# Optimization experiments

Hardware: AMD Instinct MI355X
Metric: run time of the kernel (lower is better)

The kernel has to match this reference:

```python
import jax, jax.numpy as jnp
import numpy as np

NUM_EXPERTS = 8
TOP_K = 2

def setup_inputs() -> dict:
    key = jax.random.key(0)
    k1, k2, k3, k4 = jax.random.split(key, 4)
    B, T, C, F = 4, 2048, 1024, 4096
    x = jax.random.normal(k1, (B, T, C), dtype=jnp.float32)
    gate_w = jax.random.normal(k2, (C, NUM_EXPERTS), dtype=jnp.float32) * 0.02
    w1 = jax.random.normal(k3, (NUM_EXPERTS, C, F), dtype=jnp.float32) * 0.02
    w2 = jax.random.normal(k4, (NUM_EXPERTS, F, C), dtype=jnp.float32) * 0.02
    return {"x": x, "gate_w": gate_w, "w1": w1, "w2": w2}

def reference(x, gate_w, w1, w2):
    # Router: softmax over experts, then top-k and renormalize
    router_logits = jnp.einsum('btc,ce->bte', x, gate_w)          # [B,T,E]
    routing = jax.nn.softmax(router_logits, axis=-1)
    topw, topi = jax.lax.top_k(routing, TOP_K)                    # [B,T,K]
    topw = topw / jnp.sum(topw, axis=-1, keepdims=True)
    # Combined per-expert weight per token (zero if not selected)
    onehot = jax.nn.one_hot(topi, NUM_EXPERTS, dtype=x.dtype)     # [B,T,K,E]
    combine = jnp.einsum('btk,btke->bte', topw, onehot)           # [B,T,E]
    # Expert FFNs (exact GELU, matching torch nn.GELU default)
    out = jnp.zeros_like(x)
    for e in range(NUM_EXPERTS):
        h = jax.nn.gelu(jnp.einsum('btc,cf->btf', x, w1[e]), approximate=False)
        y = jnp.einsum('btf,fc->btc', h, w2[e])
        out = out + combine[..., e:e+1] * y
    return out
```

## Files before the change

kernel.cpp:

```cpp
#include <hip/hip_runtime.h>
#include <hip/hip_bf16.h>
#include <math.h>

#define NUM_EXPERTS 8
#define NTOK 8192
#define CDIM 1024
#define FDIM 4096
#define MAXSLOTS 17408
#define MAXTILES 136

typedef __bf16 bf16x8 __attribute__((ext_vector_type(8)));
typedef float  f32x4  __attribute__((ext_vector_type(4)));

#define GPTR(p) ((const __attribute__((address_space(1))) unsigned int*)(p))
#define LPTR(p) ((__attribute__((address_space(3))) unsigned int*)(p))

__device__ __forceinline__ float gelu_exact(float v){
  return 0.5f * v * (1.0f + erff(v * 0.70710678118654752f));
}

__global__ __launch_bounds__(256) void moe_router(
    const float* __restrict__ x, const float* __restrict__ gw,
    int2* __restrict__ topi, float2* __restrict__ topw, int* __restrict__ counts)
{
  int token = blockIdx.x * 4 + (threadIdx.x >> 6);
  int lane  = threadIdx.x & 63;
  int e = lane & 7, part = lane >> 3;
  const float* xr = x + (size_t)token * CDIM;
  float s = 0.f;
  int c0 = part * 128;
  for (int c = c0; c < c0 + 128; ++c) s += xr[c] * gw[c * 8 + e];
  s += __shfl_xor(s, 8); s += __shfl_xor(s, 16); s += __shfl_xor(s, 32);
  float m1 = s; int i1 = e;
  for (int off = 1; off < 8; off <<= 1){
    float ov = __shfl_xor(m1, off); int oi = __shfl_xor(i1, off);
    if (ov > m1 || (ov == m1 && oi < i1)){ m1 = ov; i1 = oi; }
  }
  float l2 = (e == i1) ? -INFINITY : s;
  float m2 = l2; int i2 = e;
  for (int off = 1; off < 8; off <<= 1){
    float ov = __shfl_xor(m2, off); int oi = __shfl_xor(i2, off);
    if (ov > m2 || (ov == m2 && oi < i2)){ m2 = ov; i2 = oi; }
  }
  if (lane == 0){
    float r = expf(m2 - m1);
    float wa = 1.f / (1.f + r);
    topi[token] = make_int2(i1, i2);
    topw[token] = make_float2(wa, 1.f - wa);
    atomicAdd(&counts[i1], 1);
    atomicAdd(&counts[i2], 1);
  }
}

__global__ __launch_bounds__(256) void convert_x_kernel(
    const float* __restrict__ x, __hip_bfloat16* __restrict__ xb)
{
  int i = (blockIdx.x * 256 + threadIdx.x) * 4;
  float4 v = *(const float4*)(x + i);
  union { __hip_bfloat16 hh[4]; ushort4 u; } cv;
  cv.hh[0] = __float2bfloat16(v.x);
  cv.hh[1] = __float2bfloat16(v.y);
  cv.hh[2] = __float2bfloat16(v.z);
  cv.hh[3] = __float2bfloat16(v.w);
  *(ushort4*)(xb + i) = cv.u;
}

__global__ __launch_bounds__(256) void transpose_bf16_kernel(
    const float* __restrict__ in, __hip_bfloat16* __restrict__ outp, int R, int Cc)
{
  __shared__ float tile[32][33];
  const size_t msz = (size_t)R * Cc;
  const float* inm = in + (size_t)blockIdx.z * msz;
  __hip_bfloat16* outm = outp + (size_t)blockIdx.z * msz;
  int r0 = blockIdx.y * 32, c0 = blockIdx.x * 32;
  int tx = threadIdx.x, ty = threadIdx.y;
  for (int yy = 0; yy < 32; yy += 8)
    tile[ty + yy][tx] = inm[(size_t)(r0 + ty + yy) * Cc + c0 + tx];
  __syncthreads();
  for (int yy = 0; yy < 32; yy += 8)
    outm[(size_t)(c0 + ty + yy) * R + r0 + tx] = __float2bfloat16(tile[tx][ty + yy]);
}

__global__ void scan_kernel(const int* __restrict__ counts, int* cursors, int* num_tiles,
    int* tile_expert, int* tile_slotbase, int* slot_token, float* slot_weight)
{
  int t = threadIdx.x;
  if (t == 0){
    int base = 0, T = 0;
    for (int e = 0; e < NUM_EXPERTS; ++e){
      cursors[e] = base;
      int nt = (counts[e] + 127) >> 7;
      for (int i = 0; i < nt; ++i){ tile_expert[T] = e; tile_slotbase[T] = base + i * 128; ++T; }
      base += nt << 7;
    }
    *num_tiles = T;
  }
  for (int i = t; i < MAXSLOTS; i += 256){ slot_token[i] = 0; slot_weight[i] = 0.f; }
}

__global__ void assign_kernel(const int2* __restrict__ topi, const float2* __restrict__ topw,
    int* cursors, int* slot_token, float* slot_weight)
{
  int token = blockIdx.x * 256 + threadIdx.x;
  int2 ii = topi[token];
  float2 ww = topw[token];
  int p0 = atomicAdd(&cursors[ii.x], 1);
  slot_token[p0] = token; slot_weight[p0] = ww.x;
  int p1 = atomicAdd(&cursors[ii.y], 1);
  slot_token[p1] = token; slot_weight[p1] = ww.y;
}

__global__ __launch_bounds__(256) void gemm1_kernel(
    const __hip_bfloat16* __restrict__ xbf, const __hip_bfloat16* __restrict__ w1t,
    __hip_bfloat16* __restrict__ h, const int* __restrict__ num_tiles,
    const int* __restrict__ tile_expert, const int* __restrict__ tile_slotbase,
    const int* __restrict__ slot_token)
{
  __shared__ __align__(16) __hip_bfloat16 As[128 * 64];
  __shared__ __align__(16) __hip_bfloat16 Bs[128 * 64];
  const int tm = blockIdx.y;
  if (tm >= *num_tiles) return;
  const int e = tile_expert[tm];
  const int sbase = tile_slotbase[tm];
  const int n0 = blockIdx.x * 128;
  const int t = threadIdx.x;
  const int cl = t & 7;
  const __hip_bfloat16* w1e = w1t + (size_t)e * FDIM * CDIM;
  const __hip_bfloat16* aptr[4];
  const __hip_bfloat16* bptr[4];
#pragma unroll
  for (int j = 0; j < 4; ++j){
    int r = j * 32 + (t >> 3);
    int cg = cl ^ (r & 7);
    int tok = slot_token[sbase + r];
    aptr[j] = xbf + (size_t)tok * CDIM + cg * 8;
    bptr[j] = w1e + (size_t)(n0 + r) * CDIM + cg * 8;
  }
  char* asml = (char*)As + t * 16;
  char* bsml = (char*)Bs + t * 16;

  f32x4 acc[4][4] = {};
  const int lane = t & 63, wv = t >> 6;
  const int wm = (wv >> 1) * 64, wn = (wv & 1) * 64;
  const int lrow = lane & 15, quad = lane >> 4;

  for (int k0 = 0; k0 < CDIM; k0 += 64){
    __syncthreads();
#pragma unroll
    for (int j = 0; j < 4; ++j){
      __builtin_amdgcn_global_load_lds(GPTR(aptr[j] + k0), LPTR(asml + j * 4096), 16, 0, 0);
      __builtin_amdgcn_global_load_lds(GPTR(bptr[j] + k0), LPTR(bsml + j * 4096), 16, 0, 0);
    }
    __syncthreads();
#pragma unroll
    for (int kk = 0; kk < 2; ++kk){
      bf16x8 af[4], bfr[4];
#pragma unroll
      for (int i = 0; i < 4; ++i){
        int ar = wm + i * 16 + lrow;
        int ac = (kk * 4 + quad) ^ (ar & 7);
        af[i] = *(const bf16x8*)((const char*)As + ar * 128 + ac * 16);
        int br = wn + i * 16 + lrow;
        int bc = (kk * 4 + quad) ^ (br & 7);
        bfr[i] = *(const bf16x8*)((const char*)Bs + br * 128 + bc * 16);
      }
#pragma unroll
      for (int i = 0; i < 4; ++i)
#pragma unroll
        for (int j = 0; j < 4; ++j)
          acc[i][j] = __builtin_amdgcn_mfma_f32_16x16x32_bf16(af[i], bfr[j], acc[i][j], 0, 0, 0);
    }
  }
#pragma unroll
  for (int i = 0; i < 4; ++i){
#pragma unroll
    for (int r = 0; r < 4; ++r){
      int row = wm + i * 16 + quad * 4 + r;
      __hip_bfloat16* hrow = h + (size_t)(sbase + row) * FDIM + n0 + wn;
#pragma unroll
      for (int j = 0; j < 4; ++j)
        hrow[j * 16 + lrow] = __float2bfloat16(gelu_exact(acc[i][j][r]));
    }
  }
}

__global__ __launch_bounds__(256) void gemm2_kernel(
    const __hip_bfloat16* __restrict__ h, const __hip_bfloat16* __restrict__ w2t,
    float* __restrict__ out, const int* __restrict__ num_tiles,
    const int* __restrict__ tile_expert, const int* __restrict__ tile_slotbase,
    const int* __restrict__ slot_token, const float* __restrict__ slot_weight)
{
  __shared__ __align__(16) __hip_bfloat16 As[128 * 64];
  __shared__ __align__(16) __hip_bfloat16 Bs[128 * 64];
  const int tm = blockIdx.y;
  if (tm >= *num_tiles) return;
  const int e = tile_expert[tm];
  const int sbase = tile_slotbase[tm];
  const int n0 = blockIdx.x * 128;
  const int t = threadIdx.x;
  const int cl = t & 7;
  const __hip_bfloat16* w2e = w2t + (size_t)e * CDIM * FDIM;
  const __hip_bfloat16* aptr[4];
  const __hip_bfloat16* bptr[4];
#pragma unroll
  for (int j = 0; j < 4; ++j){
    int r = j * 32 + (t >> 3);
    int cg = cl ^ (r & 7);
    aptr[j] = h   + (size_t)(sbase + r) * FDIM + cg * 8;
    bptr[j] = w2e + (size_t)(n0 + r)   * FDIM + cg * 8;
  }
  char* asml = (char*)As + t * 16;
  char* bsml = (char*)Bs + t * 16;

  f32x4 acc[4][4] = {};
  const int lane = t & 63, wv = t >> 6;
  const int wm = (wv >> 1) * 64, wn = (wv & 1) * 64;
  const int lrow = lane & 15, quad = lane >> 4;

  for (int k0 = 0; k0 < FDIM; k0 += 64){
    __syncthreads();
#pragma unroll
    for (int j = 0; j < 4; ++j){
      __builtin_amdgcn_global_load_lds(GPTR(aptr[j] + k0), LPTR(asml + j * 4096), 16, 0, 0);
      __builtin_amdgcn_global_load_lds(GPTR(bptr[j] + k0), LPTR(bsml + j * 4096), 16, 0, 0);
    }
    __syncthreads();
#pragma unroll
    for (int kk = 0; kk < 2; ++kk){
      bf16x8 af[4], bfr[4];
#pragma unroll
      for (int i = 0; i < 4; ++i){
        int ar = wm + i * 16 + lrow;
        int ac = (kk * 4 + quad) ^ (ar & 7);
        af[i] = *(const bf16x8*)((const char*)As + ar * 128 + ac * 16);
        int br = wn + i * 16 + lrow;
        int bc = (kk * 4 + quad) ^ (br & 7);
        bfr[i] = *(const bf16x8*)((const char*)Bs + br * 128 + bc * 16);
      }
#pragma unroll
      for (int i = 0; i < 4; ++i)
#pragma unroll
        for (int j = 0; j < 4; ++j)
          acc[i][j] = __builtin_amdgcn_mfma_f32_16x16x32_bf16(af[i], bfr[j], acc[i][j], 0, 0, 0);
    }
  }
#pragma unroll
  for (int i = 0; i < 4; ++i){
#pragma unroll
    for (int r = 0; r < 4; ++r){
      int row = wm + i * 16 + quad * 4 + r;
      int slot = sbase + row;
      int tok = slot_token[slot];
      float wgt = slot_weight[slot];
      float* orow = out + (size_t)tok * CDIM + n0 + wn;
#pragma unroll
      for (int j = 0; j < 4; ++j)
        atomicAdd(&orow[j * 16 + lrow], wgt * acc[i][j][r]);
    }
  }
}

__global__ __launch_bounds__(256) void naive_kernel(
    const float* __restrict__ x, const float* __restrict__ w1, const float* __restrict__ w2,
    const int2* __restrict__ topi, const float2* __restrict__ topw, float* __restrict__ out)
{
  __shared__ float xs[CDIM];
  __shared__ float hs[FDIM];
  int token = blockIdx.x;
  int t = threadIdx.x;
  for (int i = t; i < CDIM; i += 256) xs[i] = x[(size_t)token * CDIM + i];
  float acc[4] = {0.f, 0.f, 0.f, 0.f};
  int2 ei = topi[token]; float2 ew = topw[token];
  int elist[2] = {ei.x, ei.y}; float wlist[2] = {ew.x, ew.y};
  for (int kk = 0; kk < 2; ++kk){
    int e = elist[kk]; float wgt = wlist[kk];
    __syncthreads();
    for (int f = t; f < FDIM; f += 256){
      const float* wcol = w1 + (size_t)e * CDIM * FDIM + f;
      float s = 0.f;
      for (int c = 0; c < CDIM; ++c) s += xs[c] * wcol[(size_t)c * FDIM];
      hs[f] = gelu_exact(s);
    }
    __syncthreads();
    for (int ii = 0; ii < 4; ++ii){
      int c = ii * 256 + t;
      const float* w2col = w2 + (size_t)e * FDIM * CDIM + c;
      float s = 0.f;
      for (int f = 0; f < FDIM; ++f) s += hs[f] * w2col[(size_t)f * CDIM];
      acc[ii] += wgt * s;
    }
  }
  for (int ii = 0; ii < 4; ++ii) out[(size_t)token * CDIM + ii * 256 + t] = acc[ii];
}

extern "C" void kernel_launch(void* const* d_in, const int* in_sizes, int n_in,
                              void* d_out, int out_size, void* d_ws, size_t ws_size,
                              hipStream_t stream)
{
  const float* x  = (const float*)d_in[0];
  const float* gw = (const float*)d_in[1];
  const float* w1 = (const float*)d_in[2];
  const float* w2 = (const float*)d_in[3];
  float* out = (float*)d_out;
  char* ws = (char*)d_ws;

  int*    counts        = (int*)(ws + 0);
  int*    cursors       = (int*)(ws + 32);
  int*    num_tiles     = (int*)(ws + 64);
  int*    tile_expert   = (int*)(ws + 256);
  int*    tile_slotbase = (int*)(ws + 1024);
  int2*   topi          = (int2*)(ws + 4096);
  float2* topw          = (float2*)(ws + 4096 + 65536);
  int*    slot_token    = (int*)(ws + 135168);
  float*  slot_weight   = (float*)(ws + 204800);
  const size_t XBF_OFF = 1u << 20;
  const size_t W1T_OFF = XBF_OFF + (size_t)NTOK * CDIM * 2;
  const size_t W2T_OFF = W1T_OFF + (size_t)NUM_EXPERTS * CDIM * FDIM * 2;
  const size_t H_OFF   = W2T_OFF + (size_t)NUM_EXPERTS * CDIM * FDIM * 2;
  const size_t NEED    = H_OFF + (size_t)MAXSLOTS * FDIM * 2;
  __hip_bfloat16* xbf = (__hip_bfloat16*)(ws + XBF_OFF);
  __hip_bfloat16* w1t = (__hip_bfloat16*)(ws + W1T_OFF);
  __hip_bfloat16* w2t = (__hip_bfloat16*)(ws + W2T_OFF);
  __hip_bfloat16* h   = (__hip_bfloat16*)(ws + H_OFF);

  hipMemsetAsync(ws, 0, 4096, stream);
  hipMemsetAsync(d_out, 0, (size_t)out_size * sizeof(float), stream);

  moe_router<<<NTOK / 4, 256, 0, stream>>>(x, gw, topi, topw, counts);

  if (ws_size >= NEED){
    convert_x_kernel<<<NTOK * CDIM / (4 * 256), 256, 0, stream>>>(x, xbf);
    transpose_bf16_kernel<<<dim3(FDIM / 32, CDIM / 32, NUM_EXPERTS), dim3(32, 8), 0, stream>>>(w1, w1t, CDIM, FDIM);
    transpose_bf16_kernel<<<dim3(CDIM / 32, FDIM / 32, NUM_EXPERTS), dim3(32, 8), 0, stream>>>(w2, w2t, FDIM, CDIM);
    scan_kernel<<<1, 256, 0, stream>>>(counts, cursors, num_tiles, tile_expert, tile_slotbase, slot_token, slot_weight);
    assign_kernel<<<NTOK / 256, 256, 0, stream>>>(topi, topw, cursors, slot_token, slot_weight);
    gemm1_kernel<<<dim3(FDIM / 128, MAXTILES), 256, 0, stream>>>(xbf, w1t, h, num_tiles, tile_expert, tile_slotbase, slot_token);
    gemm2_kernel<<<dim3(CDIM / 128, MAXTILES), 256, 0, stream>>>(h, w2t, out, num_tiles, tile_expert, tile_slotbase, slot_token, slot_weight);
  } else {
    naive_kernel<<<NTOK, 256, 0, stream>>>(x, w1, w2, topi, topw, out);
  }
}
```

Measured before the change: 1.188 ms.

## Remap GEMM blocks per XCD for L2 locality and split-K the second GEMM

Both grouped GEMMs now use a 1D grid and decode the block index so that each XCD (blocks are dispatched round-robin across the 8 XCDs) processes a contiguous range of 17 M-tiles. That range tends to share one expert's weights, which should improve L2 reuse within each XCD. The second GEMM also splits K in two, doubling its block count from 8 column tiles per M-tile to 16, for better CU occupancy. The cost is that each output element now receives twice as many float atomic adds.

```diff
diff --git a/kernel.cpp b/kernel.cpp
--- a/kernel.cpp
+++ b/kernel.cpp
@@ -8,6 +8,7 @@
 #define FDIM 4096
 #define MAXSLOTS 17408
 #define MAXTILES 136
+#define TILES_PER_XCD 17
 
 typedef __bf16 bf16x8 __attribute__((ext_vector_type(8)));
 typedef float  f32x4  __attribute__((ext_vector_type(4)));
@@ -118,23 +119,28 @@
 {
   __shared__ __align__(16) __hip_bfloat16 As[128 * 64];
   __shared__ __align__(16) __hip_bfloat16 Bs[128 * 64];
-  const int tm = blockIdx.y;
+  const int L = blockIdx.x;
+  const int xcd = L & 7;
+  const int j = L >> 3;
+  const int tl = j >> 5;
+  const int nb = j & 31;
+  const int tm = xcd * TILES_PER_XCD + tl;
   if (tm >= *num_tiles) return;
   const int e = tile_expert[tm];
   const int sbase = tile_slotbase[tm];
-  const int n0 = blockIdx.x * 128;
+  const int n0 = nb * 128;
   const int t = threadIdx.x;
   const int cl = t & 7;
   const __hip_bfloat16* w1e = w1t + (size_t)e * FDIM * CDIM;
   const __hip_bfloat16* aptr[4];
   const __hip_bfloat16* bptr[4];
 #pragma unroll
-  for (int j = 0; j < 4; ++j){
-    int r = j * 32 + (t >> 3);
+  for (int jj = 0; jj < 4; ++jj){
+    int r = jj * 32 + (t >> 3);
     int cg = cl ^ (r & 7);
     int tok = slot_token[sbase + r];
-    aptr[j] = xbf + (size_t)tok * CDIM + cg * 8;
-    bptr[j] = w1e + (size_t)(n0 + r) * CDIM + cg * 8;
+    aptr[jj] = xbf + (size_t)tok * CDIM + cg * 8;
+    bptr[jj] = w1e + (size_t)(n0 + r) * CDIM + cg * 8;
   }
   char* asml = (char*)As + t * 16;
   char* bsml = (char*)Bs + t * 16;
@@ -147,9 +153,9 @@
   for (int k0 = 0; k0 < CDIM; k0 += 64){
     __syncthreads();
 #pragma unroll
-    for (int j = 0; j < 4; ++j){
-      __builtin_amdgcn_global_load_lds(GPTR(aptr[j] + k0), LPTR(asml + j * 4096), 16, 0, 0);
-      __builtin_amdgcn_global_load_lds(GPTR(bptr[j] + k0), LPTR(bsml + j * 4096), 16, 0, 0);
+    for (int jj = 0; jj < 4; ++jj){
+      __builtin_amdgcn_global_load_lds(GPTR(aptr[jj] + k0), LPTR(asml + jj * 4096), 16, 0, 0);
+      __builtin_amdgcn_global_load_lds(GPTR(bptr[jj] + k0), LPTR(bsml + jj * 4096), 16, 0, 0);
     }
     __syncthreads();
 #pragma unroll
@@ -167,8 +173,8 @@
 #pragma unroll
       for (int i = 0; i < 4; ++i)
 #pragma unroll
-        for (int j = 0; j < 4; ++j)
-          acc[i][j] = __builtin_amdgcn_mfma_f32_16x16x32_bf16(af[i], bfr[j], acc[i][j], 0, 0, 0);
+        for (int jj = 0; jj < 4; ++jj)
+          acc[i][jj] = __builtin_amdgcn_mfma_f32_16x16x32_bf16(af[i], bfr[jj], acc[i][jj], 0, 0, 0);
     }
   }
 #pragma unroll
@@ -178,8 +184,8 @@
       int row = wm + i * 16 + quad * 4 + r;
       __hip_bfloat16* hrow = h + (size_t)(sbase + row) * FDIM + n0 + wn;
 #pragma unroll
-      for (int j = 0; j < 4; ++j)
-        hrow[j * 16 + lrow] = __float2bfloat16(gelu_exact(acc[i][j][r]));
+      for (int jj = 0; jj < 4; ++jj)
+        hrow[jj * 16 + lrow] = __float2bfloat16(gelu_exact(acc[i][jj][r]));
     }
   }
 }
@@ -192,22 +198,28 @@
 {
   __shared__ __align__(16) __hip_bfloat16 As[128 * 64];
   __shared__ __align__(16) __hip_bfloat16 Bs[128 * 64];
-  const int tm = blockIdx.y;
+  const int L = blockIdx.x;
+  const int xcd = L & 7;
+  const int j = L >> 3;
+  const int tl = j >> 4;
+  const int nb = (j >> 1) & 7;
+  const int ks = j & 1;
+  const int tm = xcd * TILES_PER_XCD + tl;
   if (tm >= *num_tiles) return;
   const int e = tile_expert[tm];
   const int sbase = tile_slotbase[tm];
-  const int n0 = blockIdx.x * 128;
+  const int n0 = nb * 128;
   const int t = threadIdx.x;
   const int cl = t & 7;
   const __hip_bfloat16* w2e = w2t + (size_t)e * CDIM * FDIM;
   const __hip_bfloat16* aptr[4];
   const __hip_bfloat16* bptr[4];
 #pragma unroll
-  for (int j = 0; j < 4; ++j){
-    int r = j * 32 + (t >> 3);
+  for (int jj = 0; jj < 4; ++jj){
+    int r = jj * 32 + (t >> 3);
     int cg = cl ^ (r & 7);
-    aptr[j] = h   + (size_t)(sbase + r) * FDIM + cg * 8;
-    bptr[j] = w2e + (size_t)(n0 + r)   * FDIM + cg * 8;
+    aptr[jj] = h   + (size_t)(sbase + r) * FDIM + cg * 8;
+    bptr[jj] = w2e + (size_t)(n0 + r)   * FDIM + cg * 8;
   }
   char* asml = (char*)As + t * 16;
   char* bsml = (char*)Bs + t * 16;
@@ -217,12 +229,13 @@
   const int wm = (wv >> 1) * 64, wn = (wv & 1) * 64;
   const int lrow = lane & 15, quad = lane >> 4;
 
-  for (int k0 = 0; k0 < FDIM; k0 += 64){
-    __syncthreads();
-#pragma unroll
-    for (int j = 0; j < 4; ++j){
-      __builtin_amdgcn_global_load_lds(GPTR(aptr[j] + k0), LPTR(asml + j * 4096), 16, 0, 0);
-      __builtin_amdgcn_global_load_lds(GPTR(bptr[j] + k0), LPTR(bsml + j * 4096), 16, 0, 0);
+  const int kbeg = ks * (FDIM / 2);
+  for (int k0 = kbeg; k0 < kbeg + FDIM / 2; k0 += 64){
+    __syncthreads();
+#pragma unroll
+    for (int jj = 0; jj < 4; ++jj){
+      __builtin_amdgcn_global_load_lds(GPTR(aptr[jj] + k0), LPTR(asml + jj * 4096), 16, 0, 0);
+      __builtin_amdgcn_global_load_lds(GPTR(bptr[jj] + k0), LPTR(bsml + jj * 4096), 16, 0, 0);
     }
     __syncthreads();
 #pragma unroll
@@ -240,8 +253,8 @@
 #pragma unroll
       for (int i = 0; i < 4; ++i)
 #pragma unroll
-        for (int j = 0; j < 4; ++j)
-          acc[i][j] = __builtin_amdgcn_mfma_f32_16x16x32_bf16(af[i], bfr[j], acc[i][j], 0, 0, 0);
+        for (int jj = 0; jj < 4; ++jj)
+          acc[i][jj] = __builtin_amdgcn_mfma_f32_16x16x32_bf16(af[i], bfr[jj], acc[i][jj], 0, 0, 0);
     }
   }
 #pragma unroll
@@ -254,8 +267,8 @@
       float wgt = slot_weight[slot];
       float* orow = out + (size_t)tok * CDIM + n0 + wn;
 #pragma unroll
-      for (int j = 0; j < 4; ++j)
-        atomicAdd(&orow[j * 16 + lrow], wgt * acc[i][j][r]);
+      for (int jj = 0; jj < 4; ++jj)
+        atomicAdd(&orow[jj * 16 + lrow], wgt * acc[i][jj][r]);
     }
   }
 }
@@ -334,8 +347,8 @@
     transpose_bf16_kernel<<<dim3(CDIM / 32, FDIM / 32, NUM_EXPERTS), dim3(32, 8), 0, stream>>>(w2, w2t, FDIM, CDIM);
     scan_kernel<<<1, 256, 0, stream>>>(counts, cursors, num_tiles, tile_expert, tile_slotbase, slot_token, slot_weight);
     assign_kernel<<<NTOK / 256, 256, 0, stream>>>(topi, topw, cursors, slot_token, slot_weight);
-    gemm1_kernel<<<dim3(FDIM / 128, MAXTILES), 256, 0, stream>>>(xbf, w1t, h, num_tiles, tile_expert, tile_slotbase, slot_token);
-    gemm2_kernel<<<dim3(CDIM / 128, MAXTILES), 256, 0, stream>>>(h, w2t, out, num_tiles, tile_expert, tile_slotbase, slot_token, slot_weight);
+    gemm1_kernel<<<8 * TILES_PER_XCD * 32, 256, 0, stream>>>(xbf, w1t, h, num_tiles, tile_expert, tile_slotbase, slot_token);
+    gemm2_kernel<<<8 * TILES_PER_XCD * 8 * 2, 256, 0, stream>>>(h, w2t, out, num_tiles, tile_expert, tile_slotbase, slot_token, slot_weight);
   } else {
     naive_kernel<<<NTOK, 256, 0, stream>>>(x, w1, w2, topi, topw, out);
   }
```

New measurement: 1.210 ms. About the same (+1.8%).
